# Kernel tuning notes

Measured on AMD Instinct MI355X. Metric: run time of the kernel, lower is better.

Reference implementation:

```python
import jax, jax.numpy as jnp
import numpy as np
import math

D_MODEL = 1024
N_HEADS = 16
HEAD_DIM = D_MODEL // N_HEADS
B, T = 2, 2048


def _rope(q, k):
    # q, k: (B, H, T, Dh)
    Dh = q.shape[-1]
    Tq = q.shape[2]
    dim = jnp.arange(0, Dh, 2, dtype=jnp.float32)
    inv_freq = 1.0 / (10000.0 ** (dim / Dh))
    pos = jnp.arange(Tq, dtype=jnp.float32)
    freqs = pos[:, None] * inv_freq[None, :]          # (T, Dh/2)
    sin = jnp.sin(freqs)[None, None]                  # (1,1,T,Dh/2)
    cos = jnp.cos(freqs)[None, None]

    def rot(t):
        te, to = t[..., ::2], t[..., 1::2]
        re = te * cos - to * sin
        ro = te * sin + to * cos
        return jnp.stack([re, ro], axis=-1).reshape(t.shape)

    return rot(q), rot(k)


def setup_inputs() -> dict:
    key = jax.random.key(0)
    ks = jax.random.split(key, 4)
    std = 1.0 / math.sqrt(D_MODEL)
    x = jax.random.normal(ks[0], (B, T, D_MODEL), dtype=jnp.float32)
    W_qkv = jax.random.normal(ks[1], (D_MODEL, 3 * D_MODEL), dtype=jnp.float32) * std
    b_qkv = jnp.zeros((3 * D_MODEL,), dtype=jnp.float32)
    W_out = jax.random.normal(ks[2], (D_MODEL, D_MODEL), dtype=jnp.float32) * std
    b_out = jnp.zeros((D_MODEL,), dtype=jnp.float32)
    attention_mask = jnp.ones((B, T), dtype=jnp.int32)
    return {"x": x, "attention_mask": attention_mask, "W_qkv": W_qkv,
            "b_qkv": b_qkv, "W_out": W_out, "b_out": b_out}


def reference(x, attention_mask, W_qkv, b_qkv, W_out, b_out):
    Bx, Tx, D = x.shape
    qkv = x @ W_qkv + b_qkv                            # (B,T,3D)
    q, k, v = jnp.split(qkv, 3, axis=-1)
    # (B,T,H,Dh) -> (B,H,T,Dh)
    q = q.reshape(Bx, Tx, N_HEADS, HEAD_DIM).transpose(0, 2, 1, 3)
    k = k.reshape(Bx, Tx, N_HEADS, HEAD_DIM).transpose(0, 2, 1, 3)
    v = v.reshape(Bx, Tx, N_HEADS, HEAD_DIM).transpose(0, 2, 1, 3)
    q, k = _rope(q, k)
    scale = 1.0 / math.sqrt(float(HEAD_DIM))
    scores = jnp.einsum('bhqd,bhkd->bhqk', q, k) * scale
    causal = jnp.tril(jnp.ones((Tx, Tx), dtype=bool))[None, None]
    pad = attention_mask.astype(bool)[:, None, None, :]
    mask = causal & pad
    scores = jnp.where(mask, scores, -jnp.inf)
    probs = jax.nn.softmax(scores, axis=-1)
    out = jnp.einsum('bhqk,bhkd->bhqd', probs, v)      # (B,H,T,Dh)
    out = out.transpose(0, 2, 1, 3).reshape(Bx, Tx, D)
    return out @ W_out + b_out
```

## Files before the change

### kernel.cpp

```cpp
#include <hip/hip_runtime.h>
#include <math.h>
#include <stdint.h>

#define D_MODEL 1024
#define N_HEADS 16
#define HEAD_DIM 64
#define BATCH 2
#define SEQ 2048
#define TOKENS (BATCH * SEQ)

typedef __attribute__((ext_vector_type(8))) short short8;
typedef __attribute__((ext_vector_type(8))) _Float16 half8;
typedef __attribute__((ext_vector_type(4))) float floatx4;

#define BMFMA(a, b, c) __builtin_amdgcn_mfma_f32_16x16x32_bf16(a, b, c, 0, 0, 0)
#define HMFMA(a, b, c) __builtin_amdgcn_mfma_f32_16x16x32_f16(a, b, c, 0, 0, 0)

__device__ __forceinline__ unsigned short f2bf(float f) {
    uint32_t u = __float_as_uint(f);
    u += 0x7fffu + ((u >> 16) & 1u);
    return (unsigned short)(u >> 16);
}
__device__ __forceinline__ float bf2f(unsigned short h) {
    return __uint_as_float(((uint32_t)h) << 16);
}
__device__ __forceinline__ unsigned short f2h(float f) {
    union { _Float16 h; unsigned short u; } cv;
    cv.h = (_Float16)f;
    return cv.u;
}
__device__ __forceinline__ float h2f(unsigned short u) {
    union { unsigned short u; _Float16 h; } cv;
    cv.u = u;
    return (float)cv.h;
}
__device__ __forceinline__ void ld16h(const unsigned short* p, float* f) {
    uint4 u0 = *(const uint4*)p;
    uint4 u1 = *(const uint4*)(p + 8);
    const uint32_t* a = (const uint32_t*)&u0;
    const uint32_t* b = (const uint32_t*)&u1;
#pragma unroll
    for (int j = 0; j < 4; ++j) {
        f[2 * j]     = h2f((unsigned short)(a[j] & 0xffffu));
        f[2 * j + 1] = h2f((unsigned short)(a[j] >> 16));
        f[8 + 2 * j]     = h2f((unsigned short)(b[j] & 0xffffu));
        f[8 + 2 * j + 1] = h2f((unsigned short)(b[j] >> 16));
    }
}

#define GLD_LDS16(gp, lp) __builtin_amdgcn_global_load_lds(                 \
    (const __attribute__((address_space(1))) void*)(gp),                    \
    (__attribute__((address_space(3))) void*)(lp), 16, 0, 0)

__global__ __launch_bounds__(256) void split_inputs(
    const float* __restrict__ X, const float* __restrict__ Wqkv,
    const float* __restrict__ Wout, const int* __restrict__ am,
    unsigned short* __restrict__ Axh, unsigned short* __restrict__ Bt,
    unsigned short* __restrict__ Bt2, unsigned long long* __restrict__ mbits,
    float2* __restrict__ tab)
{
    __shared__ float t[32][33];
    const int tid = threadIdx.x;
    const int bid = blockIdx.x;
    if (bid < 2048) {
        const int idx = bid * 2048 + tid * 8;
        const int row = idx >> 10;
        const int c = idx & 1023;
        float4 v0 = *(const float4*)(X + (size_t)row * 1024 + c);
        float4 v1 = *(const float4*)(X + (size_t)row * 1024 + c + 4);
        float f[8] = {v0.x, v0.y, v0.z, v0.w, v1.x, v1.y, v1.z, v1.w};
        uint32_t p[4];
#pragma unroll
        for (int j = 0; j < 4; ++j)
            p[j] = (uint32_t)f2h(f[2 * j]) | ((uint32_t)f2h(f[2 * j + 1]) << 16);
        *(uint4*)(Axh + (size_t)row * 1024 + c) = *(uint4*)p;
    } else if (bid < 5120) {
        const int id = bid - 2048;
        const int n0 = (id % 96) * 32, k0 = (id / 96) * 32;
        const int c = tid & 31, r = tid >> 5;
#pragma unroll
        for (int i = 0; i < 4; ++i)
            t[r + 8 * i][c] = Wqkv[(size_t)(k0 + r + 8 * i) * 3072 + n0 + c];
        __syncthreads();
#pragma unroll
        for (int i = 0; i < 4; ++i) {
            int dn = r + 8 * i;
            Bt[(size_t)(n0 + dn) * 1024 + k0 + c] = f2h(t[c][dn]);
        }
    } else if (bid < 6144) {
        const int id = bid - 5120;
        const int n0 = (id & 31) * 32, k0 = (id >> 5) * 32;
        const int c = tid & 31, r = tid >> 5;
#pragma unroll
        for (int i = 0; i < 4; ++i)
            t[r + 8 * i][c] = Wout[(size_t)(k0 + r + 8 * i) * 1024 + n0 + c];
        __syncthreads();
#pragma unroll
        for (int i = 0; i < 4; ++i) {
            int dn = r + 8 * i;
            Bt2[(size_t)(n0 + dn) * 1024 + k0 + c] = f2h(t[c][dn]);
        }
    } else if (bid == 6144) {
        if (tid < 64) {
            const int* a = am + tid * 64;
            unsigned long long m = 0ull;
            for (int j = 0; j < 64; ++j)
                m |= (unsigned long long)(a[j] != 0 ? 1u : 0u) << j;
            mbits[tid] = m;
        }
    } else {
        const int i = bid - 6145;
#pragma unroll
        for (int e = 0; e < 16; ++e) {
            int idx = i * 4096 + e * 256 + tid;
            int tt = idx >> 5, pr = idx & 31;
            double ex = (double)(2 * pr) / 64.0;
            float inv = (float)exp2(-ex * 13.287712379549449);
            float ang = (float)tt * inv;
            float s, c;
            __sincosf(ang, &s, &c);
            tab[idx] = make_float2(c, s);
        }
    }
}

template<int WM, int WN, int FM, int FN, int OUT16>
__global__ __launch_bounds__(256) void gemm_mfma_h(
    const unsigned short* __restrict__ A, int lda,
    const unsigned short* __restrict__ Bt, int ldb,
    const float* __restrict__ bias, void* __restrict__ Cv, int ldc, int nTiles)
{
    constexpr int BM = WM * FM * 16;
    constexpr int BN = WN * FN * 16;
    constexpr int NA = BM / 64;
    constexpr int NB = BN / 64;

    __shared__ __align__(16) unsigned short sA0[BM * 32];
    __shared__ __align__(16) unsigned short sA1[BM * 32];
    __shared__ __align__(16) unsigned short sB0[BN * 32];
    __shared__ __align__(16) unsigned short sB1[BN * 32];

    const int tid = threadIdx.x;
    const int w = tid >> 6, lane = tid & 63;
    const int l15 = lane & 15, quad = lane >> 4;
    const int wm = w / WN, wn = w % WN;

    const int lin = blockIdx.x;
    const int msuper = lin / (8 * nTiles);
    const int rem = lin % (8 * nTiles);
    const int m0 = (msuper * 8 + (rem & 7)) * BM;
    const int n0 = (rem >> 3) * BN;

    const int ch = (lane & 3) ^ ((lane >> 3) & 3);
    const int sw = (quad ^ ((l15 >> 1) & 3)) * 8;

    const unsigned short* aG[NA];
    const unsigned short* bG[NB];
#pragma unroll
    for (int i = 0; i < NA; ++i)
        aG[i] = A + (size_t)(m0 + (w * NA + i) * 16 + (lane >> 2)) * lda + ch * 8;
#pragma unroll
    for (int i = 0; i < NB; ++i)
        bG[i] = Bt + (size_t)(n0 + (w * NB + i) * 16 + (lane >> 2)) * ldb + ch * 8;

    floatx4 acc[FM][FN];
#pragma unroll
    for (int fm = 0; fm < FM; ++fm)
#pragma unroll
        for (int fn = 0; fn < FN; ++fn) acc[fm][fn] = (floatx4)0.f;

    for (int ks = 0; ks < 16; ++ks) {
        const int ko = ks * 64;
        __syncthreads();
#pragma unroll
        for (int i = 0; i < NA; ++i) {
            GLD_LDS16(aG[i] + ko,      sA0 + (w * NA + i) * 512);
            GLD_LDS16(aG[i] + ko + 32, sA1 + (w * NA + i) * 512);
        }
#pragma unroll
        for (int i = 0; i < NB; ++i) {
            GLD_LDS16(bG[i] + ko,      sB0 + (w * NB + i) * 512);
            GLD_LDS16(bG[i] + ko + 32, sB1 + (w * NB + i) * 512);
        }
        __syncthreads();

        half8 a0[FM], a1[FM], b0[FN], b1[FN];
#pragma unroll
        for (int fm = 0; fm < FM; ++fm) {
            const int off = ((wm * FM + fm) * 16 + l15) * 32 + sw;
            a0[fm] = *(const half8*)&sA0[off];
            a1[fm] = *(const half8*)&sA1[off];
        }
#pragma unroll
        for (int fn = 0; fn < FN; ++fn) {
            const int off = ((wn * FN + fn) * 16 + l15) * 32 + sw;
            b0[fn] = *(const half8*)&sB0[off];
            b1[fn] = *(const half8*)&sB1[off];
        }
#pragma unroll
        for (int fm = 0; fm < FM; ++fm)
#pragma unroll
            for (int fn = 0; fn < FN; ++fn) {
                floatx4 a = acc[fm][fn];
                a = HMFMA(a0[fm], b0[fn], a);
                a = HMFMA(a1[fm], b1[fn], a);
                acc[fm][fn] = a;
            }
    }

#pragma unroll
    for (int fm = 0; fm < FM; ++fm)
#pragma unroll
        for (int fn = 0; fn < FN; ++fn) {
            int col = n0 + (wn * FN + fn) * 16 + l15;
            float bv = bias[col];
#pragma unroll
            for (int r = 0; r < 4; ++r) {
                int row = m0 + (wm * FM + fm) * 16 + quad * 4 + r;
                if (OUT16) {
                    ((unsigned short*)Cv)[(size_t)row * ldc + col] =
                        f2h(acc[fm][fn][r] + bv);
                } else {
                    ((float*)Cv)[(size_t)row * ldc + col] =
                        acc[fm][fn][r] + bv;
                }
            }
        }
}

__global__ __launch_bounds__(256) void prep_qkv(
    const unsigned short* __restrict__ qkvh, const float2* __restrict__ tab,
    unsigned short* __restrict__ Qh, unsigned short* __restrict__ Kh,
    unsigned short* __restrict__ Vh)
{
    __shared__ float vt[64][65];
    const int tid = threadIdx.x;
    const int lin = blockIdx.x;
    const int tt = lin & 31, bh = lin >> 5;
    const int b = bh >> 4, h = bh & 15;
    const int r = tid >> 2;
    const int dblk = (tid & 3) * 16;
    const int tg = tt * 64 + r;
    const size_t src = (size_t)(b * SEQ + tg) * 3072 + h * 64 + dblk;
    const size_t dst = ((size_t)bh * SEQ + tg) * 64 + dblk;

    float q[16], k[16], v[16];
    ld16h(qkvh + src, q);
    ld16h(qkvh + src + 1024, k);
    ld16h(qkvh + src + 2048, v);

    float2 cs[8];
#pragma unroll
    for (int i = 0; i < 4; ++i)
        *(float4*)&cs[2 * i] = *(const float4*)(tab + (size_t)tg * 32
                                                + (dblk >> 1) + 2 * i);
#pragma unroll
    for (int j = 0; j < 16; j += 2) {
        float c = cs[j >> 1].x, s = cs[j >> 1].y;
        float qe = q[j], qo = q[j + 1];
        q[j] = qe * c - qo * s; q[j + 1] = qe * s + qo * c;
        float ke = k[j], ko = k[j + 1];
        k[j] = ke * c - ko * s; k[j + 1] = ke * s + ko * c;
    }
    uint32_t ph[8];
#pragma unroll
    for (int j = 0; j < 8; ++j) {
        float f0 = q[2 * j] * 0.125f, f1 = q[2 * j + 1] * 0.125f;
        ph[j] = (uint32_t)f2h(f0) | ((uint32_t)f2h(f1) << 16);
    }
    *(uint4*)(Qh + dst) = *(uint4*)&ph[0]; *(uint4*)(Qh + dst + 8) = *(uint4*)&ph[4];
#pragma unroll
    for (int j = 0; j < 8; ++j)
        ph[j] = (uint32_t)f2h(k[2 * j]) | ((uint32_t)f2h(k[2 * j + 1]) << 16);
    *(uint4*)(Kh + dst) = *(uint4*)&ph[0]; *(uint4*)(Kh + dst + 8) = *(uint4*)&ph[4];

#pragma unroll
    for (int j = 0; j < 16; ++j) vt[r][dblk + j] = v[j];
    __syncthreads();
    const int d2 = tid >> 2;
    const int tb = (tid & 3) * 16;
#pragma unroll
    for (int j = 0; j < 8; ++j) {
        float f0 = vt[tb + 2 * j][d2], f1 = vt[tb + 2 * j + 1][d2];
        ph[j] = (uint32_t)f2bf(f0) | ((uint32_t)f2bf(f1) << 16);
    }
    const size_t vdst = ((size_t)bh * 64 + d2) * SEQ + tt * 64 + tb;
    *(uint4*)(Vh + vdst) = *(uint4*)&ph[0]; *(uint4*)(Vh + vdst + 8) = *(uint4*)&ph[4];
}

__global__ __launch_bounds__(256, 6) void flash_mfma(
    const unsigned short* __restrict__ Qh, const unsigned short* __restrict__ Kh,
    const unsigned short* __restrict__ Vh,
    const unsigned long long* __restrict__ mbits,
    unsigned short* __restrict__ attnx,
    float* __restrict__ Opart, float* __restrict__ lpart)
{
    __shared__ __align__(16) unsigned short sK[4096];
    __shared__ __align__(16) unsigned short sV[4096];
    __shared__ __align__(16) unsigned short sP[4096];

    const int tid = threadIdx.x;
    const int lane = tid & 63, w = tid >> 6;
    const int l15 = lane & 15, quad = lane >> 4;
    const int lin0 = blockIdx.x;
    const int xcd = lin0 & 7, idx = lin0 >> 3;
    const int bh = xcd * 4 + (idx & 3);
    const int rank = idx >> 2;
    int qt, k0, kend, mode;
    if (rank < 16)        { qt = 16 + rank; k0 = 0;  kend = 15; mode = 1; }
    else {
        const int i = (rank - 16) >> 1;
        if ((rank & 1) == 0) { qt = 31 - i; k0 = 16; kend = qt; mode = 2; }
        else                 { qt = 15 - i; k0 = 0;  kend = qt; mode = 0; }
    }
    const int b = bh >> 4, h = bh & 15;
    const int sw = (quad ^ ((l15 >> 1) & 3)) * 8;
    const int ch = (lane & 3) ^ ((lane >> 3) & 3);
    unsigned short* pbase = sP + w * 1024;

    short8 ones;
#pragma unroll
    for (int jj = 0; jj < 8; ++jj) ones[jj] = (short)0x3F80;

    const size_t qb = ((size_t)bh * SEQ + qt * 64 + w * 16 + l15) * 64 + quad * 8;
    const half8 qh0 = *(const half8*)(Qh + qb);
    const half8 qh1 = *(const half8*)(Qh + qb + 32);

    unsigned int mlo = 0xffffffffu, mhi = 0xffffffffu;
    if (lane < 32) {
        unsigned long long mw = mbits[b * 32 + lane];
        mlo = (unsigned int)mw;
        mhi = (unsigned int)(mw >> 32);
    }
    const bool fullmask =
        (__ballot((mlo & mhi) == 0xffffffffu) == ~0ull);

    const size_t kRow0 = ((size_t)bh * SEQ + w * 16 + (lane >> 2)) * 64 + ch * 8;
    const size_t vRow  = ((size_t)bh * 64 + w * 16 + (lane >> 2)) * SEQ + ch * 8;

    floatx4 O[4];
    floatx4 lAcc = (floatx4)0.f;
#pragma unroll
    for (int nf = 0; nf < 4; ++nf) O[nf] = (floatx4)0.f;

    const int mg = qt * 64 + w * 16 + l15;

    for (int kt = k0; kt <= kend; ++kt) {
        __syncthreads();
        {
            const size_t kg = kRow0 + (size_t)kt * 64 * 64;
            const size_t vg = vRow + (size_t)kt * 64;
            GLD_LDS16(Kh + kg,      sK + w * 512);
            GLD_LDS16(Kh + kg + 32, sK + 2048 + w * 512);
            GLD_LDS16(Vh + vg,      sV + w * 512);
            GLD_LDS16(Vh + vg + 32, sV + 2048 + w * 512);
        }
        __syncthreads();

        const bool diag = (kt == qt);
        unsigned int wlo = 0xffffffffu, whi = 0xffffffffu;
        if (!fullmask) {
            wlo = (unsigned int)__shfl((int)mlo, kt);
            whi = (unsigned int)__shfl((int)mhi, kt);
        }

#pragma unroll
        for (int nf = 0; nf < 4; ++nf) {
            const int base = (nf * 16 + l15) * 32 + sw;
            const half8 k0v = *(const half8*)&sK[base];
            const half8 k1v = *(const half8*)&sK[2048 + base];
            floatx4 s = (floatx4)0.f;
            s = HMFMA(k0v, qh0, s);
            s = HMFMA(k1v, qh1, s);

            float pv[4];
            if (fullmask && !diag) {
#pragma unroll
                for (int r = 0; r < 4; ++r)
                    pv[r] = __expf(s[r] - 16.0f);
            } else {
                const int tb = kt * 64 + nf * 16 + quad * 4;
                const unsigned int msel = (nf & 2) ? whi : wlo;
                const int p4 = (nf & 1) * 16 + quad * 4;
#pragma unroll
                for (int r = 0; r < 4; ++r) {
                    bool ok = ((msel >> (p4 + r)) & 1u) != 0u;
                    if (diag) ok = ok && (tb + r <= mg);
                    pv[r] = ok ? __expf(s[r] - 16.0f) : 0.0f;
                }
            }
            uint32_t w0, w1;
            asm("v_cvt_pk_bf16_f32 %0, %1, %2" : "=v"(w0) : "v"(pv[0]), "v"(pv[1]));
            asm("v_cvt_pk_bf16_f32 %0, %1, %2" : "=v"(w1) : "v"(pv[2]), "v"(pv[3]));
            const int pos = (((nf & 1) * 2 + (quad >> 1)) ^ ((l15 >> 1) & 3));
            *(uint2*)(pbase + (nf >> 1) * 512 + l15 * 32 + pos * 8
                      + (quad & 1) * 4) = make_uint2(w0, w1);
        }

        const short8 pf0 = *(const short8*)(pbase + l15 * 32 + sw);
        const short8 pf1 = *(const short8*)(pbase + 512 + l15 * 32 + sw);

        lAcc = BMFMA(pf0, ones, lAcc);
        lAcc = BMFMA(pf1, ones, lAcc);
#pragma unroll
        for (int nf = 0; nf < 4; ++nf) {
            const int vb = (nf * 16 + l15) * 32 + sw;
            floatx4 o = O[nf];
            o = BMFMA(pf0, *(const short8*)&sV[vb], o);
            o = BMFMA(pf1, *(const short8*)&sV[2048 + vb], o);
            O[nf] = o;
        }
    }

    if (mode == 0) {
        float rl[4];
#pragma unroll
        for (int r = 0; r < 4; ++r) rl[r] = 1.0f / lAcc[r];
#pragma unroll
        for (int nf = 0; nf < 4; ++nf)
#pragma unroll
            for (int r = 0; r < 4; ++r) {
                const int tok = b * SEQ + qt * 64 + w * 16 + quad * 4 + r;
                const int col = h * 64 + nf * 16 + l15;
                attnx[(size_t)tok * 1024 + col] = f2h(O[nf][r] * rl[r]);
            }
    } else {
        const int qt16 = qt - 16;
        float* Op = Opart + ((mode == 2) ? 2097152 : 0)
                  + (((size_t)bh * 16 + qt16) * 64) * 64;
#pragma unroll
        for (int nf = 0; nf < 4; ++nf)
#pragma unroll
            for (int r = 0; r < 4; ++r)
                Op[(w * 16 + quad * 4 + r) * 64 + nf * 16 + l15] = O[nf][r];
        if (l15 == 0) {
            float* lp = lpart + ((mode == 2) ? 32768 : 0)
                      + (bh * 16 + qt16) * 64;
#pragma unroll
            for (int r = 0; r < 4; ++r)
                lp[w * 16 + quad * 4 + r] = lAcc[r];
        }
    }
}

__global__ __launch_bounds__(256) void flash_merge(
    const float* __restrict__ Opart, const float* __restrict__ lpart,
    unsigned short* __restrict__ attnx)
{
    const int bh = blockIdx.x >> 4, qt16 = blockIdx.x & 15;
    const int b = bh >> 4, h = bh & 15;
    const int tid = threadIdx.x;
    const int q = tid >> 2, dblk = (tid & 3) * 16;
    const size_t ob = (((size_t)bh * 16 + qt16) * 64 + q) * 64 + dblk;
    const int lb = (bh * 16 + qt16) * 64 + q;
    const float rl = 1.0f / (lpart[lb] + lpart[lb + 32768]);

    uint32_t ph[8];
#pragma unroll
    for (int i = 0; i < 4; ++i) {
        float4 a = *(const float4*)(Opart + ob + 4 * i);
        float4 c = *(const float4*)(Opart + ob + 2097152 + 4 * i);
        float f0 = (a.x + c.x) * rl, f1 = (a.y + c.y) * rl;
        float f2 = (a.z + c.z) * rl, f3 = (a.w + c.w) * rl;
        ph[2 * i]     = (uint32_t)f2h(f0) | ((uint32_t)f2h(f1) << 16);
        ph[2 * i + 1] = (uint32_t)f2h(f2) | ((uint32_t)f2h(f3) << 16);
    }
    const int tok = b * SEQ + (16 + qt16) * 64 + q;
    unsigned short* dst = attnx + (size_t)tok * 1024 + h * 64 + dblk;
    *(uint4*)dst = *(uint4*)&ph[0];
    *(uint4*)(dst + 8) = *(uint4*)&ph[4];
}

extern "C" void kernel_launch(void* const* d_in, const int* in_sizes, int n_in,
                              void* d_out, int out_size, void* d_ws, size_t ws_size,
                              hipStream_t stream)
{
    const float* x    = (const float*)d_in[0];
    const int*   am   = (const int*)d_in[1];
    const float* Wqkv = (const float*)d_in[2];
    const float* bqkv = (const float*)d_in[3];
    const float* Wout = (const float*)d_in[4];
    const float* bout = (const float*)d_in[5];
    float* out = (float*)d_out;

    char* ws = (char*)d_ws;
    unsigned short* Bt  = (unsigned short*)ws;
    unsigned short* Bt2 = (unsigned short*)(ws + 6291456);
    float2* tab = (float2*)(ws + 8388608);
    unsigned long long* mbits = (unsigned long long*)(ws + 8912896);
    unsigned short* qkvh = (unsigned short*)(ws + 12582912);
    unsigned short* attnx = qkvh;
    unsigned short* Qh = (unsigned short*)(ws + 62914560);
    unsigned short* Kh = (unsigned short*)(ws + 71303168);
    unsigned short* Vh = (unsigned short*)(ws + 79691776);
    unsigned short* Axh = (unsigned short*)(ws + 88080384);
    float* Opart = (float*)(ws + 88080384);
    float* lpart = (float*)(ws + 104857600);

    split_inputs<<<6161, 256, 0, stream>>>(x, Wqkv, Wout, am,
                                           Axh, Bt, Bt2, mbits, tab);

    gemm_mfma_h<2, 2, 4, 4, 1><<<768, 256, 0, stream>>>(
        Axh, 1024, Bt, 1024, bqkv, qkvh, 3072, 24);

    prep_qkv<<<1024, 256, 0, stream>>>(qkvh, tab, Qh, Kh, Vh);

    flash_mfma<<<1536, 256, 0, stream>>>(Qh, Kh, Vh, mbits, attnx,
                                         Opart, lpart);
    flash_merge<<<512, 256, 0, stream>>>(Opart, lpart, attnx);

    gemm_mfma_h<2, 2, 4, 4, 0><<<256, 256, 0, stream>>>(
        attnx, 1024, Bt2, 1024, bout, out, 1024, 8);
}
```

Before: 192.2 us.

## Fuse RoPE, Q scaling and V transpose into the QKV GEMM epilogue

Replaces the QKV GEMM plus the separate prep_qkv kernel with a single GEMM. Its epilogue adds bias, applies rotary embedding using lane shuffles to pair even/odd columns, scales Q, and writes Q/K in fp16 head-major layout and V transposed in bf16. This removes the intermediate fp16 qkv buffer round trip and one kernel launch. The tradeoff is narrower, more scattered stores in the epilogue and extra table loads per element.

```diff
diff --git a/kernel.cpp b/kernel.cpp
--- a/kernel.cpp
+++ b/kernel.cpp
@@ -33,19 +33,6 @@
     union { unsigned short u; _Float16 h; } cv;
     cv.u = u;
     return (float)cv.h;
-}
-__device__ __forceinline__ void ld16h(const unsigned short* p, float* f) {
-    uint4 u0 = *(const uint4*)p;
-    uint4 u1 = *(const uint4*)(p + 8);
-    const uint32_t* a = (const uint32_t*)&u0;
-    const uint32_t* b = (const uint32_t*)&u1;
-#pragma unroll
-    for (int j = 0; j < 4; ++j) {
-        f[2 * j]     = h2f((unsigned short)(a[j] & 0xffffu));
-        f[2 * j + 1] = h2f((unsigned short)(a[j] >> 16));
-        f[8 + 2 * j]     = h2f((unsigned short)(b[j] & 0xffffu));
-        f[8 + 2 * j + 1] = h2f((unsigned short)(b[j] >> 16));
-    }
 }
 
 #define GLD_LDS16(gp, lp) __builtin_amdgcn_global_load_lds(                 \
@@ -124,11 +111,132 @@
     }
 }
 
-template<int WM, int WN, int FM, int FN, int OUT16>
+__global__ __launch_bounds__(256) void gemm_qkv_fused(
+    const unsigned short* __restrict__ Axh, const unsigned short* __restrict__ Bt,
+    const float* __restrict__ bias, const float2* __restrict__ tab,
+    unsigned short* __restrict__ Qh, unsigned short* __restrict__ Kh,
+    unsigned short* __restrict__ Vh)
+{
+    __shared__ __align__(16) unsigned short sA0[4096], sA1[4096];
+    __shared__ __align__(16) unsigned short sB0[4096], sB1[4096];
+
+    const int tid = threadIdx.x;
+    const int w = tid >> 6, lane = tid & 63;
+    const int l15 = lane & 15, quad = lane >> 4;
+    const int wm = w >> 1, wn = w & 1;
+
+    const int lin = blockIdx.x;
+    const int msuper = lin / 192;
+    const int rem = lin % 192;
+    const int m0 = (msuper * 8 + (rem & 7)) * 128;
+    const int n0 = (rem >> 3) * 128;
+
+    const int ch = (lane & 3) ^ ((lane >> 3) & 3);
+    const int sw = (quad ^ ((l15 >> 1) & 3)) * 8;
+
+    const unsigned short* aG[2];
+    const unsigned short* bG[2];
+#pragma unroll
+    for (int i = 0; i < 2; ++i) {
+        aG[i] = Axh + (size_t)(m0 + (w * 2 + i) * 16 + (lane >> 2)) * 1024 + ch * 8;
+        bG[i] = Bt + (size_t)(n0 + (w * 2 + i) * 16 + (lane >> 2)) * 1024 + ch * 8;
+    }
+
+    floatx4 acc[4][4];
+#pragma unroll
+    for (int fm = 0; fm < 4; ++fm)
+#pragma unroll
+        for (int fn = 0; fn < 4; ++fn) acc[fm][fn] = (floatx4)0.f;
+
+    for (int ks = 0; ks < 16; ++ks) {
+        const int ko = ks * 64;
+        __syncthreads();
+#pragma unroll
+        for (int i = 0; i < 2; ++i) {
+            GLD_LDS16(aG[i] + ko,      sA0 + (w * 2 + i) * 512);
+            GLD_LDS16(aG[i] + ko + 32, sA1 + (w * 2 + i) * 512);
+            GLD_LDS16(bG[i] + ko,      sB0 + (w * 2 + i) * 512);
+            GLD_LDS16(bG[i] + ko + 32, sB1 + (w * 2 + i) * 512);
+        }
+        __syncthreads();
+
+        half8 a0[4], a1[4], b0[4], b1[4];
+#pragma unroll
+        for (int fm = 0; fm < 4; ++fm) {
+            const int off = ((wm * 4 + fm) * 16 + l15) * 32 + sw;
+            a0[fm] = *(const half8*)&sA0[off];
+            a1[fm] = *(const half8*)&sA1[off];
+        }
+#pragma unroll
+        for (int fn = 0; fn < 4; ++fn) {
+            const int off = ((wn * 4 + fn) * 16 + l15) * 32 + sw;
+            b0[fn] = *(const half8*)&sB0[off];
+            b1[fn] = *(const half8*)&sB1[off];
+        }
+#pragma unroll
+        for (int fm = 0; fm < 4; ++fm)
+#pragma unroll
+            for (int fn = 0; fn < 4; ++fn) {
+                floatx4 a = acc[fm][fn];
+                a = HMFMA(a0[fm], b0[fn], a);
+                a = HMFMA(a1[fm], b1[fn], a);
+                acc[fm][fn] = a;
+            }
+    }
+
+    if (n0 < 2048) {
+        const bool isQ = (n0 < 1024);
+        unsigned short* dst = isQ ? Qh : Kh;
+        const float qs = isQ ? 0.125f : 1.0f;
+#pragma unroll
+        for (int fm = 0; fm < 4; ++fm)
+#pragma unroll
+            for (int fn = 0; fn < 4; ++fn) {
+                const int col = n0 + (wn * 4 + fn) * 16 + l15;
+                const int hcol = col & 1023;
+                const int hh = hcol >> 6, d = hcol & 63;
+                const int pr = d >> 1;
+                const bool odd = (d & 1) != 0;
+                const float bv = bias[col];
+#pragma unroll
+                for (int r = 0; r < 4; ++r) {
+                    const int row = m0 + (wm * 4 + fm) * 16 + quad * 4 + r;
+                    const int tg = row & 2047, bb = row >> 11;
+                    float val = acc[fm][fn][r] + bv;
+                    float part = __shfl_xor(val, 1);
+                    const float2 cs = tab[tg * 32 + pr];
+                    float res = odd ? (part * cs.y + val * cs.x)
+                                    : (val * cs.x - part * cs.y);
+                    dst[((size_t)(bb * 16 + hh) * SEQ + tg) * 64 + d] =
+                        f2h(res * qs);
+                }
+            }
+    } else {
+#pragma unroll
+        for (int fm = 0; fm < 4; ++fm)
+#pragma unroll
+            for (int fn = 0; fn < 4; ++fn) {
+                const int col = n0 + (wn * 4 + fn) * 16 + l15;
+                const int hcol = col & 1023;
+                const int hh = hcol >> 6, d = hcol & 63;
+                const float bv = bias[col];
+                const int row0 = m0 + (wm * 4 + fm) * 16 + quad * 4;
+                const int tg0 = row0 & 2047, bb = row0 >> 11;
+                uint32_t pk0 = (uint32_t)f2bf(acc[fm][fn][0] + bv)
+                             | ((uint32_t)f2bf(acc[fm][fn][1] + bv) << 16);
+                uint32_t pk1 = (uint32_t)f2bf(acc[fm][fn][2] + bv)
+                             | ((uint32_t)f2bf(acc[fm][fn][3] + bv) << 16);
+                *(uint2*)(Vh + ((size_t)(bb * 16 + hh) * 64 + d) * SEQ + tg0) =
+                    make_uint2(pk0, pk1);
+            }
+    }
+}
+
+template<int WM, int WN, int FM, int FN>
 __global__ __launch_bounds__(256) void gemm_mfma_h(
     const unsigned short* __restrict__ A, int lda,
     const unsigned short* __restrict__ Bt, int ldb,
-    const float* __restrict__ bias, void* __restrict__ Cv, int ldc, int nTiles)
+    const float* __restrict__ bias, float* __restrict__ C, int ldc, int nTiles)
 {
     constexpr int BM = WM * FM * 16;
     constexpr int BN = WN * FN * 16;
@@ -217,75 +325,9 @@
 #pragma unroll
             for (int r = 0; r < 4; ++r) {
                 int row = m0 + (wm * FM + fm) * 16 + quad * 4 + r;
-                if (OUT16) {
-                    ((unsigned short*)Cv)[(size_t)row * ldc + col] =
-                        f2h(acc[fm][fn][r] + bv);
-                } else {
-                    ((float*)Cv)[(size_t)row * ldc + col] =
-                        acc[fm][fn][r] + bv;
-                }
-            }
-        }
-}
-
-__global__ __launch_bounds__(256) void prep_qkv(
-    const unsigned short* __restrict__ qkvh, const float2* __restrict__ tab,
-    unsigned short* __restrict__ Qh, unsigned short* __restrict__ Kh,
-    unsigned short* __restrict__ Vh)
-{
-    __shared__ float vt[64][65];
-    const int tid = threadIdx.x;
-    const int lin = blockIdx.x;
-    const int tt = lin & 31, bh = lin >> 5;
-    const int b = bh >> 4, h = bh & 15;
-    const int r = tid >> 2;
-    const int dblk = (tid & 3) * 16;
-    const int tg = tt * 64 + r;
-    const size_t src = (size_t)(b * SEQ + tg) * 3072 + h * 64 + dblk;
-    const size_t dst = ((size_t)bh * SEQ + tg) * 64 + dblk;
-
-    float q[16], k[16], v[16];
-    ld16h(qkvh + src, q);
-    ld16h(qkvh + src + 1024, k);
-    ld16h(qkvh + src + 2048, v);
-
-    float2 cs[8];
-#pragma unroll
-    for (int i = 0; i < 4; ++i)
-        *(float4*)&cs[2 * i] = *(const float4*)(tab + (size_t)tg * 32
-                                                + (dblk >> 1) + 2 * i);
-#pragma unroll
-    for (int j = 0; j < 16; j += 2) {
-        float c = cs[j >> 1].x, s = cs[j >> 1].y;
-        float qe = q[j], qo = q[j + 1];
-        q[j] = qe * c - qo * s; q[j + 1] = qe * s + qo * c;
-        float ke = k[j], ko = k[j + 1];
-        k[j] = ke * c - ko * s; k[j + 1] = ke * s + ko * c;
-    }
-    uint32_t ph[8];
-#pragma unroll
-    for (int j = 0; j < 8; ++j) {
-        float f0 = q[2 * j] * 0.125f, f1 = q[2 * j + 1] * 0.125f;
-        ph[j] = (uint32_t)f2h(f0) | ((uint32_t)f2h(f1) << 16);
-    }
-    *(uint4*)(Qh + dst) = *(uint4*)&ph[0]; *(uint4*)(Qh + dst + 8) = *(uint4*)&ph[4];
-#pragma unroll
-    for (int j = 0; j < 8; ++j)
-        ph[j] = (uint32_t)f2h(k[2 * j]) | ((uint32_t)f2h(k[2 * j + 1]) << 16);
-    *(uint4*)(Kh + dst) = *(uint4*)&ph[0]; *(uint4*)(Kh + dst + 8) = *(uint4*)&ph[4];
-
-#pragma unroll
-    for (int j = 0; j < 16; ++j) vt[r][dblk + j] = v[j];
-    __syncthreads();
-    const int d2 = tid >> 2;
-    const int tb = (tid & 3) * 16;
-#pragma unroll
-    for (int j = 0; j < 8; ++j) {
-        float f0 = vt[tb + 2 * j][d2], f1 = vt[tb + 2 * j + 1][d2];
-        ph[j] = (uint32_t)f2bf(f0) | ((uint32_t)f2bf(f1) << 16);
-    }
-    const size_t vdst = ((size_t)bh * 64 + d2) * SEQ + tt * 64 + tb;
-    *(uint4*)(Vh + vdst) = *(uint4*)&ph[0]; *(uint4*)(Vh + vdst + 8) = *(uint4*)&ph[4];
+                C[(size_t)row * ldc + col] = acc[fm][fn][r] + bv;
+            }
+        }
 }
 
 __global__ __launch_bounds__(256, 6) void flash_mfma(
@@ -488,8 +530,7 @@
     unsigned short* Bt2 = (unsigned short*)(ws + 6291456);
     float2* tab = (float2*)(ws + 8388608);
     unsigned long long* mbits = (unsigned long long*)(ws + 8912896);
-    unsigned short* qkvh = (unsigned short*)(ws + 12582912);
-    unsigned short* attnx = qkvh;
+    unsigned short* attnx = (unsigned short*)(ws + 12582912);
     unsigned short* Qh = (unsigned short*)(ws + 62914560);
     unsigned short* Kh = (unsigned short*)(ws + 71303168);
     unsigned short* Vh = (unsigned short*)(ws + 79691776);
@@ -500,15 +541,12 @@
     split_inputs<<<6161, 256, 0, stream>>>(x, Wqkv, Wout, am,
                                            Axh, Bt, Bt2, mbits, tab);
 
-    gemm_mfma_h<2, 2, 4, 4, 1><<<768, 256, 0, stream>>>(
-        Axh, 1024, Bt, 1024, bqkv, qkvh, 3072, 24);
-
-    prep_qkv<<<1024, 256, 0, stream>>>(qkvh, tab, Qh, Kh, Vh);
+    gemm_qkv_fused<<<768, 256, 0, stream>>>(Axh, Bt, bqkv, tab, Qh, Kh, Vh);
 
     flash_mfma<<<1536, 256, 0, stream>>>(Qh, Kh, Vh, mbits, attnx,
                                          Opart, lpart);
     flash_merge<<<512, 256, 0, stream>>>(Opart, lpart, attnx);
 
-    gemm_mfma_h<2, 2, 4, 4, 0><<<256, 256, 0, stream>>>(
+    gemm_mfma_h<2, 2, 4, 4><<<256, 256, 0, stream>>>(
         attnx, 1024, Bt2, 1024, bout, out, 1024, 8);
 }
```

Result: faster. 185.1 us (-3.7%).
